# Kernel tuning notes

Measured on AMD Instinct MI355X. Metric: run time of the kernel, lower is better.

## Reference

```python
import jax, jax.numpy as jnp
import numpy as np

V = 50257   # vocab_size
BLOCK = 1024
D = 768     # n_embd
H = 12      # n_head
L = 2       # n_layer
B = 4
T = 1024
EPS = 1e-5


def _ln(x, g, b):
    mu = jnp.mean(x, axis=-1, keepdims=True)
    var = jnp.var(x, axis=-1, keepdims=True)
    return (x - mu) * jax.lax.rsqrt(var + EPS) * g + b


def setup_inputs() -> dict:
    key = jax.random.key(0)
    ks = jax.random.split(key, 10)
    def n(k, shape, std=0.02):
        return jax.random.normal(k, shape, jnp.float32) * std
    proj_std = (2 * L) ** -0.5  # set_scale init in the torch code
    return dict(
        idx=jax.random.randint(ks[0], (B, T), 0, V),
        layer_num=0,
        wte=n(ks[1], (V, D)),
        wpe=n(ks[2], (BLOCK, D)),
        ln1_g=jnp.ones((L, D)), ln1_b=jnp.zeros((L, D)),
        attn_w=n(ks[3], (L, D, 3 * D)), attn_b=jnp.zeros((L, 3 * D)),
        proj_w=n(ks[4], (L, D, D), proj_std), proj_b=jnp.zeros((L, D)),
        ln2_g=jnp.ones((L, D)), ln2_b=jnp.zeros((L, D)),
        fc_w=n(ks[5], (L, D, 4 * D)), fc_b=jnp.zeros((L, 4 * D)),
        fc2_w=n(ks[6], (L, 4 * D, D), proj_std), fc2_b=jnp.zeros((L, D)),
        lnf_g=jnp.ones((D,)), lnf_b=jnp.zeros((D,)),
        lm_w=n(ks[7], (D, V)),
    )


def _gpt(idx, wte, wpe, ln1_g, ln1_b, attn_w, attn_b, proj_w, proj_b,
         ln2_g, ln2_b, fc_w, fc_b, fc2_w, fc2_b, lnf_g, lnf_b, lm_w):
    b, t = idx.shape
    hd = D // H
    x = wte[idx] + wpe[:t]                      # [B,T,D]
    causal = jnp.tril(jnp.ones((t, t), bool))   # [T,T]
    for l in range(L):
        h = _ln(x, ln1_g[l], ln1_b[l])
        qkv = h @ attn_w[l] + attn_b[l]          # [B,T,3D]
        q, k, v = jnp.split(qkv, 3, axis=-1)
        q = q.reshape(b, t, H, hd)
        k = k.reshape(b, t, H, hd)
        v = v.reshape(b, t, H, hd)
        att = jnp.einsum('bqhd,bkhd->bhqk', q, k) * (1.0 / np.sqrt(hd))
        att = jnp.where(causal, att, -jnp.inf)
        att = jax.nn.softmax(att, axis=-1)
        y = jnp.einsum('bhqk,bkhd->bqhd', att, v).reshape(b, t, D)
        x = x + (y @ proj_w[l] + proj_b[l])
        h2 = _ln(x, ln2_g[l], ln2_b[l])
        h2 = jax.nn.gelu(h2 @ fc_w[l] + fc_b[l], approximate=True)  # tanh GELU
        x = x + (h2 @ fc2_w[l] + fc2_b[l])
    x = _ln(x, lnf_g, lnf_b)
    return x @ lm_w                             # [B,T,V] logits


def reference(idx, layer_num, wte, wpe, ln1_g, ln1_b, attn_w, attn_b,
              proj_w, proj_b, ln2_g, ln2_b, fc_w, fc_b, fc2_w, fc2_b,
              lnf_g, lnf_b, lm_w):
    # layer_num is unused in the forward math (pipeline-stage bookkeeping)
    return _gpt(idx, wte, wpe, ln1_g, ln1_b, attn_w, attn_b, proj_w, proj_b,
                ln2_g, ln2_b, fc_w, fc_b, fc2_w, fc2_b, lnf_g, lnf_b, lm_w)
```

## Files before the change

kernel.cpp:

```cpp
#include <hip/hip_runtime.h>
#include <hip/hip_bf16.h>
#include <cstdint>
#include <cstddef>

typedef __bf16 bf16_t;
typedef __bf16 bf16x8 __attribute__((ext_vector_type(8)));
typedef float f32x4 __attribute__((ext_vector_type(4)));

#define GLB_AS(p) ((__attribute__((address_space(1))) void*)(void*)(p))
#define LDS_AS(p) ((__attribute__((address_space(3))) void*)(p))

__device__ __forceinline__ float wave_red_sum(float v) {
#pragma unroll
  for (int o = 1; o < 64; o <<= 1) v += __shfl_xor(v, o, 64);
  return v;
}

__device__ __forceinline__ float gelu_tanh(float v) {
  float c = 0.7978845608028654f * (v + 0.044715f * v * v * v);
  return 0.5f * v * (1.0f + tanhf(c));
}

__global__ __launch_bounds__(256) void embed_k(const int* __restrict__ idx,
                                               const float* __restrict__ wte,
                                               const float* __restrict__ wpe,
                                               float* __restrict__ x) {
  const int m = blockIdx.x;
  const int tid = threadIdx.x;
  const int tok = idx[m];
  const int t = m & 1023;
#pragma unroll
  for (int i = 0; i < 3; ++i) {
    const int d = tid + i * 256;
    x[(size_t)m * 768 + d] = wte[(size_t)tok * 768 + d] + wpe[(size_t)t * 768 + d];
  }
}

__global__ __launch_bounds__(256) void ln_k(const float* __restrict__ x,
                                            const float* __restrict__ g,
                                            const float* __restrict__ b,
                                            bf16_t* __restrict__ out) {
  const int row = blockIdx.x;
  const int tid = threadIdx.x;
  const float* xr = x + (size_t)row * 768;
  float v0 = xr[tid], v1 = xr[tid + 256], v2 = xr[tid + 512];
  float s = v0 + v1 + v2;
  float q = v0 * v0 + v1 * v1 + v2 * v2;
  s = wave_red_sum(s);
  q = wave_red_sum(q);
  __shared__ float sm[8];
  const int wave = tid >> 6, lane = tid & 63;
  if (lane == 0) { sm[wave] = s; sm[4 + wave] = q; }
  __syncthreads();
  s = sm[0] + sm[1] + sm[2] + sm[3];
  q = sm[4] + sm[5] + sm[6] + sm[7];
  const float mu = s * (1.0f / 768.0f);
  const float var = q * (1.0f / 768.0f) - mu * mu;
  const float rs = rsqrtf(var + 1e-5f);
  bf16_t* orow = out + (size_t)row * 768;
#pragma unroll
  for (int i = 0; i < 3; ++i) {
    const int d = tid + i * 256;
    const float v = (i == 0 ? v0 : (i == 1 ? v1 : v2));
    orow[d] = (bf16_t)((v - mu) * rs * g[d] + b[d]);
  }
}

__global__ __launch_bounds__(256) void transp_k(const float* __restrict__ W,
                                                bf16_t* __restrict__ WT,
                                                int K, int N, int Npad) {
  __shared__ float tile[32][33];
  const int n0 = blockIdx.x * 32, k0 = blockIdx.y * 32;
  const int tx = threadIdx.x, ty = threadIdx.y;
#pragma unroll
  for (int i = 0; i < 4; ++i) {
    const int k = k0 + ty + i * 8, n = n0 + tx;
    tile[ty + i * 8][tx] = (k < K && n < N) ? W[(size_t)k * N + n] : 0.0f;
  }
  __syncthreads();
#pragma unroll
  for (int i = 0; i < 4; ++i) {
    const int n = n0 + ty + i * 8, k = k0 + tx;
    if (n < Npad && k < K) WT[(size_t)n * K + k] = (bf16_t)tile[tx][ty + i * 8];
  }
}

__global__ __launch_bounds__(256) void vtr_k(const bf16_t* __restrict__ qkv,
                                             bf16_t* __restrict__ vt) {
  __shared__ bf16_t tile[64][72];
  const int bh = blockIdx.y;
  const int h = bh % 12, b = bh / 12;
  const int t0 = blockIdx.x * 64;
  const int tx = threadIdx.x & 63;
  const int wv = threadIdx.x >> 6;
#pragma unroll
  for (int i = 0; i < 16; ++i) {
    const int r = wv * 16 + i;
    tile[r][tx] = qkv[(size_t)(b * 1024 + t0 + r) * 2304 + 1536 + h * 64 + tx];
  }
  __syncthreads();
#pragma unroll
  for (int i = 0; i < 16; ++i) {
    const int d = wv * 16 + i;
    vt[((size_t)bh * 64 + d) * 1024 + t0 + tx] = tile[tx][d];
  }
}

template <int EPI>
__global__ __launch_bounds__(256) void gemm_bt(const bf16_t* __restrict__ A,
                                               const bf16_t* __restrict__ BT,
                                               const float* __restrict__ bias,
                                               void* __restrict__ outp,
                                               float* __restrict__ resid,
                                               int M, int N, int K, int Nout) {
  __shared__ __align__(16) bf16_t As[128 * 32];
  __shared__ __align__(16) bf16_t Bs[128 * 32];
  const int tid = threadIdx.x;
  const int lane = tid & 63, wave = tid >> 6;

  const int nmblk = M >> 7;
  const int nwg = gridDim.x;
  const int flat = blockIdx.x;
  const int xcd = flat & 7, rest = flat >> 3;
  const int q8 = nwg >> 3, r8 = nwg & 7;
  const int wgid = (xcd < r8 ? xcd * (q8 + 1) : r8 * (q8 + 1) + (xcd - r8) * q8) + rest;
  const int m0 = (wgid % nmblk) * 128;
  const int n0 = (wgid / nmblk) * 128;

  const int wr = wave >> 1, wc = wave & 1;
  const int fr = lane & 15, fq = lane >> 4;
  const int se = tid * 8;
  const int srow = se >> 5, scol = se & 31;
  const int wvbase = wave * 512;
  f32x4 acc[4][4] = {};

  for (int k0 = 0; k0 < K; k0 += 32) {
#pragma unroll
    for (int r = 0; r < 2; ++r) {
      __builtin_amdgcn_global_load_lds(
          GLB_AS(&A[(size_t)(m0 + srow + r * 64) * K + k0 + scol]),
          LDS_AS(&As[wvbase + r * 2048]), 16, 0, 0);
      __builtin_amdgcn_global_load_lds(
          GLB_AS(&BT[(size_t)(n0 + srow + r * 64) * K + k0 + scol]),
          LDS_AS(&Bs[wvbase + r * 2048]), 16, 0, 0);
    }
    __syncthreads();
    bf16x8 a[4], b[4];
#pragma unroll
    for (int i = 0; i < 4; ++i) {
      a[i] = *(const bf16x8*)(&As[(wr * 64 + i * 16 + fr) * 32 + fq * 8]);
      b[i] = *(const bf16x8*)(&Bs[(wc * 64 + i * 16 + fr) * 32 + fq * 8]);
    }
#pragma unroll
    for (int i = 0; i < 4; ++i)
#pragma unroll
      for (int j = 0; j < 4; ++j)
        acc[i][j] = __builtin_amdgcn_mfma_f32_16x16x32_bf16(a[i], b[j], acc[i][j], 0, 0, 0);
    __syncthreads();
  }

#pragma unroll
  for (int i = 0; i < 4; ++i) {
#pragma unroll
    for (int j = 0; j < 4; ++j) {
      const int r0 = m0 + wr * 64 + i * 16 + fq * 4;
      const int c = n0 + wc * 64 + j * 16 + fr;
      float bv = 0.0f;
      if constexpr (EPI != 3) bv = bias[c];
#pragma unroll
      for (int e = 0; e < 4; ++e) {
        const int r = r0 + e;
        float v = acc[i][j][e] + bv;
        if constexpr (EPI == 0) {
          ((bf16_t*)outp)[(size_t)r * N + c] = (bf16_t)v;
        } else if constexpr (EPI == 1) {
          ((bf16_t*)outp)[(size_t)r * N + c] = (bf16_t)gelu_tanh(v);
        } else if constexpr (EPI == 2) {
          resid[(size_t)r * N + c] += v;
        } else {
          if (c < Nout) ((float*)outp)[(size_t)r * Nout + c] = v;
        }
      }
    }
  }
}

__global__ __launch_bounds__(256) void fattn_k(const bf16_t* __restrict__ qkv,
                                               const bf16_t* __restrict__ vt,
                                               bf16_t* __restrict__ y) {
  __shared__ bf16_t Pl[4][16][40];
  const int wave = threadIdx.x >> 6, lane = threadIdx.x & 63;
  const int wid = blockIdx.x * 4 + wave;
  const int qt = wid & 63;
  const int bh = wid >> 6;
  const int h = bh % 12, b = bh / 12;
  const int fr = lane & 15, fq = lane >> 4;

  const bf16_t* qrow = qkv + (size_t)(b * 1024 + qt * 16 + fr) * 2304 + h * 64;
  const bf16x8 qf0 = *(const bf16x8*)(qrow + fq * 8);
  const bf16x8 qf1 = *(const bf16x8*)(qrow + 32 + fq * 8);

  const bf16_t* kbase = qkv + (size_t)b * 1024 * 2304 + 768 + h * 64 + fq * 8;
  const bf16_t* vbase = vt + ((size_t)bh * 64 + fr) * 1024 + fq * 8;

  f32x4 o[4] = {};
  float mrun[4], lrun[4];
#pragma unroll
  for (int e = 0; e < 4; ++e) { mrun[e] = -1e30f; lrun[e] = 0.0f; }

  const int qg = qt * 16 + fq * 4;
  const int kv_end = qt * 16 + 16;

  for (int kv0 = 0; kv0 < kv_end; kv0 += 32) {
    f32x4 s0 = {}, s1 = {};
    {
      const bf16_t* k0p = kbase + (size_t)(kv0 + fr) * 2304;
      const bf16_t* k1p = kbase + (size_t)(kv0 + 16 + fr) * 2304;
      const bf16x8 kf00 = *(const bf16x8*)(k0p);
      const bf16x8 kf01 = *(const bf16x8*)(k0p + 32);
      const bf16x8 kf10 = *(const bf16x8*)(k1p);
      const bf16x8 kf11 = *(const bf16x8*)(k1p + 32);
      s0 = __builtin_amdgcn_mfma_f32_16x16x32_bf16(qf0, kf00, s0, 0, 0, 0);
      s0 = __builtin_amdgcn_mfma_f32_16x16x32_bf16(qf1, kf01, s0, 0, 0, 0);
      s1 = __builtin_amdgcn_mfma_f32_16x16x32_bf16(qf0, kf10, s1, 0, 0, 0);
      s1 = __builtin_amdgcn_mfma_f32_16x16x32_bf16(qf1, kf11, s1, 0, 0, 0);
    }
    float v0[4], v1[4];
#pragma unroll
    for (int e = 0; e < 4; ++e) {
      v0[e] = (kv0 + fr <= qg + e) ? s0[e] * 0.125f : -1e30f;
      v1[e] = (kv0 + 16 + fr <= qg + e) ? s1[e] * 0.125f : -1e30f;
    }
    float p0[4], p1[4];
#pragma unroll
    for (int e = 0; e < 4; ++e) {
      float mx = fmaxf(v0[e], v1[e]);
      mx = fmaxf(mx, __shfl_xor(mx, 1, 64));
      mx = fmaxf(mx, __shfl_xor(mx, 2, 64));
      mx = fmaxf(mx, __shfl_xor(mx, 4, 64));
      mx = fmaxf(mx, __shfl_xor(mx, 8, 64));
      const float mnew = fmaxf(mrun[e], mx);
      p0[e] = __expf(v0[e] - mnew);
      p1[e] = __expf(v1[e] - mnew);
      float rs = p0[e] + p1[e];
      rs += __shfl_xor(rs, 1, 64);
      rs += __shfl_xor(rs, 2, 64);
      rs += __shfl_xor(rs, 4, 64);
      rs += __shfl_xor(rs, 8, 64);
      const float alpha = __expf(mrun[e] - mnew);
      lrun[e] = lrun[e] * alpha + rs;
      mrun[e] = mnew;
#pragma unroll
      for (int db = 0; db < 4; ++db) o[db][e] *= alpha;
    }
#pragma unroll
    for (int e = 0; e < 4; ++e) {
      Pl[wave][fq * 4 + e][fr] = (bf16_t)p0[e];
      Pl[wave][fq * 4 + e][16 + fr] = (bf16_t)p1[e];
    }
    asm volatile("s_waitcnt lgkmcnt(0)" ::: "memory");
    const bf16x8 pf = *(const bf16x8*)(&Pl[wave][fr][fq * 8]);
#pragma unroll
    for (int db = 0; db < 4; ++db) {
      const bf16x8 vf = *(const bf16x8*)(vbase + (size_t)db * 16 * 1024 + kv0);
      o[db] = __builtin_amdgcn_mfma_f32_16x16x32_bf16(pf, vf, o[db], 0, 0, 0);
    }
  }

#pragma unroll
  for (int db = 0; db < 4; ++db) {
#pragma unroll
    for (int e = 0; e < 4; ++e) {
      const int q = qt * 16 + fq * 4 + e;
      const int d = db * 16 + fr;
      y[(size_t)(b * 1024 + q) * 768 + h * 64 + d] = (bf16_t)(o[db][e] / lrun[e]);
    }
  }
}

extern "C" void kernel_launch(void* const* d_in, const int* in_sizes, int n_in,
                              void* d_out, int out_size, void* d_ws, size_t ws_size,
                              hipStream_t stream) {
  constexpr int Bb = 4, T = 1024, Lg = 2, Vr = 50257, Vp = 50304;
  constexpr int M = Bb * T;

  const int* idx = (const int*)d_in[0];
  const float* wte = (const float*)d_in[2];
  const float* wpe = (const float*)d_in[3];
  const float* ln1_g = (const float*)d_in[4];
  const float* ln1_b = (const float*)d_in[5];
  const float* attn_w = (const float*)d_in[6];
  const float* attn_b = (const float*)d_in[7];
  const float* proj_w = (const float*)d_in[8];
  const float* proj_b = (const float*)d_in[9];
  const float* ln2_g = (const float*)d_in[10];
  const float* ln2_b = (const float*)d_in[11];
  const float* fc_w = (const float*)d_in[12];
  const float* fc_b = (const float*)d_in[13];
  const float* fc2_w = (const float*)d_in[14];
  const float* fc2_b = (const float*)d_in[15];
  const float* lnf_g = (const float*)d_in[16];
  const float* lnf_b = (const float*)d_in[17];
  const float* lm_w = (const float*)d_in[18];
  float* out = (float*)d_out;

  char* wp = (char*)d_ws;
  auto take = [&](size_t n) { char* p = wp; wp += (n + 255) & ~(size_t)255; return p; };
  bf16_t* WqkvT = (bf16_t*)take((size_t)Lg * 2304 * 768 * 2);
  bf16_t* WprojT = (bf16_t*)take((size_t)Lg * 768 * 768 * 2);
  bf16_t* WfcT = (bf16_t*)take((size_t)Lg * 3072 * 768 * 2);
  bf16_t* Wfc2T = (bf16_t*)take((size_t)Lg * 768 * 3072 * 2);
  bf16_t* WlmT = (bf16_t*)take((size_t)Vp * 768 * 2);
  float* xb = (float*)take((size_t)M * 768 * 4);
  bf16_t* hb = (bf16_t*)take((size_t)M * 768 * 2);
  bf16_t* qkvb = (bf16_t*)take((size_t)M * 2304 * 2);
  bf16_t* yb = (bf16_t*)take((size_t)M * 768 * 2);
  bf16_t* actb = (bf16_t*)take((size_t)M * 3072 * 2);
  bf16_t* vtb = (bf16_t*)take((size_t)M * 768 * 2);

  const dim3 tb(32, 8);
  for (int l = 0; l < Lg; ++l) {
    transp_k<<<dim3(2304 / 32, 768 / 32), tb, 0, stream>>>(
        attn_w + (size_t)l * 768 * 2304, WqkvT + (size_t)l * 2304 * 768, 768, 2304, 2304);
    transp_k<<<dim3(768 / 32, 768 / 32), tb, 0, stream>>>(
        proj_w + (size_t)l * 768 * 768, WprojT + (size_t)l * 768 * 768, 768, 768, 768);
    transp_k<<<dim3(3072 / 32, 768 / 32), tb, 0, stream>>>(
        fc_w + (size_t)l * 768 * 3072, WfcT + (size_t)l * 3072 * 768, 768, 3072, 3072);
    transp_k<<<dim3(768 / 32, 3072 / 32), tb, 0, stream>>>(
        fc2_w + (size_t)l * 3072 * 768, Wfc2T + (size_t)l * 768 * 3072, 3072, 768, 768);
  }
  transp_k<<<dim3(Vp / 32, 768 / 32), tb, 0, stream>>>(lm_w, WlmT, 768, Vr, Vp);

  embed_k<<<M, 256, 0, stream>>>(idx, wte, wpe, xb);

  for (int l = 0; l < Lg; ++l) {
    ln_k<<<M, 256, 0, stream>>>(xb, ln1_g + l * 768, ln1_b + l * 768, hb);
    gemm_bt<0><<<(M / 128) * (2304 / 128), 256, 0, stream>>>(
        hb, WqkvT + (size_t)l * 2304 * 768, attn_b + l * 2304, qkvb, nullptr,
        M, 2304, 768, 2304);
    vtr_k<<<dim3(T / 64, Bb * 12), 256, 0, stream>>>(qkvb, vtb);
    fattn_k<<<(Bb * 12 * 64) / 4, 256, 0, stream>>>(qkvb, vtb, yb);
    gemm_bt<2><<<(M / 128) * (768 / 128), 256, 0, stream>>>(
        yb, WprojT + (size_t)l * 768 * 768, proj_b + l * 768, nullptr, xb,
        M, 768, 768, 768);
    ln_k<<<M, 256, 0, stream>>>(xb, ln2_g + l * 768, ln2_b + l * 768, hb);
    gemm_bt<1><<<(M / 128) * (3072 / 128), 256, 0, stream>>>(
        hb, WfcT + (size_t)l * 3072 * 768, fc_b + l * 3072, actb, nullptr,
        M, 3072, 768, 3072);
    gemm_bt<2><<<(M / 128) * (768 / 128), 256, 0, stream>>>(
        actb, Wfc2T + (size_t)l * 768 * 3072, fc2_b + l * 768, nullptr, xb,
        M, 768, 3072, 768);
  }
  ln_k<<<M, 256, 0, stream>>>(xb, lnf_g, lnf_b, hb);
  gemm_bt<3><<<(M / 128) * (Vp / 128), 256, 0, stream>>>(
      hb, WlmT, nullptr, out, nullptr, M, Vp, 768, Vr);
}
```

Baseline: 1.355 ms.

## Add persistent 256x256 GEMM with 4-stage async LDS pipeline for QKV, FC, LM head

```diff
diff --git a/kernel.cpp b/kernel.cpp
--- a/kernel.cpp
+++ b/kernel.cpp
@@ -20,6 +20,13 @@
   float c = 0.7978845608028654f * (v + 0.044715f * v * v * v);
   return 0.5f * v * (1.0f + tanhf(c));
 }
+
+__device__ __forceinline__ f32x4 mfma16(f32x4 a, f32x4 b, f32x4 c) {
+  return __builtin_amdgcn_mfma_f32_16x16x32_bf16(
+      __builtin_bit_cast(bf16x8, a), __builtin_bit_cast(bf16x8, b), c, 0, 0, 0);
+}
+
+__device__ __forceinline__ int swz(int off) { return off ^ ((off >> 3) & 0x30); }
 
 __global__ __launch_bounds__(256) void embed_k(const int* __restrict__ idx,
                                                const float* __restrict__ wte,
@@ -107,6 +114,146 @@
 }
 
 template <int EPI>
+__global__ __launch_bounds__(512, 2) void gemm256p(const bf16_t* __restrict__ A,
+                                                   const bf16_t* __restrict__ BT,
+                                                   const float* __restrict__ bias,
+                                                   void* __restrict__ outp,
+                                                   int M, int N, int K, int Nout,
+                                                   int ntiles) {
+  __shared__ __align__(16) char lds[131072];
+  const int tid = threadIdx.x;
+  const int lane = tid & 63, wave = tid >> 6;
+  const int wr = wave >> 2, wc = wave & 3;
+  const int fr = lane & 15, fq = lane >> 4;
+
+  const int nmblk = M >> 8;
+  const int G = gridDim.x;
+  const int flat = blockIdx.x;
+  const int xcd = flat & 7, rest = flat >> 3;
+  const int q8 = G >> 3, r8 = G & 7;
+  const int bid = (xcd < r8 ? xcd * (q8 + 1) : r8 * (q8 + 1) + (xcd - r8) * q8) + rest;
+  const int qt = ntiles / G, rt = ntiles % G;
+  const int tstart = bid * qt + (bid < rt ? bid : rt);
+  const int cnt = qt + (bid < rt ? 1 : 0);
+  if (cnt == 0) return;
+  const int NT = K >> 5;
+  const int gEnd = cnt * NT;
+
+  int srow[2], scb[2];
+#pragma unroll
+  for (int u = 0; u < 2; ++u) {
+    const int s = swz(u * 8192 + tid * 16);
+    srow[u] = s >> 6;
+    scb[u] = s & 63;
+  }
+  const char* Abase = (const char*)A;
+  const char* Bbase = (const char*)BT;
+
+  auto stage4 = [&](int buf, int m0x, int n0x, int tauK) {
+#pragma unroll
+    for (int u = 0; u < 2; ++u) {
+      const char* srcA = Abase + ((size_t)(m0x + srow[u]) * K + tauK * 32) * 2 + scb[u];
+      __builtin_amdgcn_global_load_lds(GLB_AS(srcA),
+          LDS_AS(&lds[buf * 32768 + u * 8192 + wave * 1024]), 16, 0, 0);
+      const char* srcB = Bbase + ((size_t)(n0x + srow[u]) * K + tauK * 32) * 2 + scb[u];
+      __builtin_amdgcn_global_load_lds(GLB_AS(srcB),
+          LDS_AS(&lds[buf * 32768 + 16384 + u * 8192 + wave * 1024]), 16, 0, 0);
+    }
+  };
+
+  const int swzA0 = swz((wr * 128 + fr) * 64 + fq * 16);
+  const int swzB0 = 16384 + swz((wc * 64 + fr) * 64 + fq * 16);
+
+  int m0 = (tstart % nmblk) << 8, n0 = (tstart / nmblk) << 8;
+  int m3 = m0, n3 = n0, t3;
+  auto adv = [&](int& mx, int& nx, int& tx) {
+    if (++tx == NT) { tx = 0; mx += 256; if (mx >= M) { mx = 0; nx += 256; } }
+  };
+
+  f32x4 acc[8][4] = {};
+  f32x4 Xa[8], Xb[4], Ya[8], Yb[4];
+
+  {
+    int ms = m0, ns = n0, ts = 0;
+    stage4(0, ms, ns, ts); adv(ms, ns, ts);
+    stage4(1, ms, ns, ts); adv(ms, ns, ts);
+    stage4(2, ms, ns, ts); adv(ms, ns, ts);
+    m3 = ms; n3 = ns; t3 = ts;
+  }
+  asm volatile("s_waitcnt vmcnt(8)" ::: "memory");
+  __builtin_amdgcn_s_barrier();
+  __builtin_amdgcn_sched_barrier(0);
+#pragma unroll
+  for (int i = 0; i < 8; ++i) Xa[i] = *(const f32x4*)(&lds[swzA0 + i * 1024]);
+#pragma unroll
+  for (int j = 0; j < 4; ++j) Xb[j] = *(const f32x4*)(&lds[swzB0 + j * 1024]);
+
+  int g = 0;
+
+#define GSTEP(CA, CB, NA, NB)                                                          \
+  {                                                                                    \
+    if (g + 2 < gEnd) { asm volatile("s_waitcnt vmcnt(4)" ::: "memory"); }             \
+    else              { asm volatile("s_waitcnt vmcnt(0)" ::: "memory"); }             \
+    __builtin_amdgcn_s_barrier();                                                      \
+    __builtin_amdgcn_sched_barrier(0);                                                 \
+    if (g + 1 < gEnd) {                                                                \
+      const int bb1 = ((g + 1) & 3) << 15;                                             \
+      _Pragma("unroll")                                                                \
+      for (int i = 0; i < 8; ++i) NA[i] = *(const f32x4*)(&lds[bb1 + swzA0 + i * 1024]); \
+      _Pragma("unroll")                                                                \
+      for (int j = 0; j < 4; ++j) NB[j] = *(const f32x4*)(&lds[bb1 + swzB0 + j * 1024]); \
+      asm volatile("s_waitcnt lgkmcnt(12)" ::: "memory");                              \
+    } else {                                                                           \
+      asm volatile("s_waitcnt lgkmcnt(0)" ::: "memory");                               \
+    }                                                                                  \
+    __builtin_amdgcn_sched_barrier(0);                                                 \
+    if (g + 3 < gEnd) { stage4((g + 3) & 3, m3, n3, t3); adv(m3, n3, t3); }            \
+    __builtin_amdgcn_s_setprio(1);                                                     \
+    _Pragma("unroll")                                                                  \
+    for (int i = 0; i < 8; ++i)                                                        \
+      _Pragma("unroll")                                                                \
+      for (int j = 0; j < 4; ++j) acc[i][j] = mfma16(CA[i], CB[j], acc[i][j]);         \
+    __builtin_amdgcn_s_setprio(0);                                                     \
+    ++g;                                                                               \
+  }
+
+  for (int t = 0; t < cnt; ++t) {
+    for (int k2 = 0; k2 < NT; k2 += 2) {
+      GSTEP(Xa, Xb, Ya, Yb);
+      GSTEP(Ya, Yb, Xa, Xb);
+    }
+#pragma unroll
+    for (int i8 = 0; i8 < 8; ++i8) {
+#pragma unroll
+      for (int j4 = 0; j4 < 4; ++j4) {
+        const int r0 = m0 + wr * 128 + i8 * 16 + fq * 4;
+        const int c = n0 + wc * 64 + j4 * 16 + fr;
+        float bv = 0.0f;
+        if constexpr (EPI != 3) bv = bias[c];
+#pragma unroll
+        for (int e = 0; e < 4; ++e) {
+          const int r = r0 + e;
+          float v = acc[i8][j4][e] + bv;
+          if constexpr (EPI == 0) {
+            ((bf16_t*)outp)[(size_t)r * N + c] = (bf16_t)v;
+          } else if constexpr (EPI == 1) {
+            ((bf16_t*)outp)[(size_t)r * N + c] = (bf16_t)gelu_tanh(v);
+          } else {
+            if (c < Nout) ((float*)outp)[(size_t)r * Nout + c] = v;
+          }
+        }
+      }
+    }
+#pragma unroll
+    for (int i8 = 0; i8 < 8; ++i8)
+#pragma unroll
+      for (int j4 = 0; j4 < 4; ++j4) acc[i8][j4] = (f32x4){0.0f, 0.0f, 0.0f, 0.0f};
+    m0 += 256; if (m0 >= M) { m0 = 0; n0 += 256; }
+  }
+#undef GSTEP
+}
+
+template <int EPI>
 __global__ __launch_bounds__(256) void gemm_bt(const bf16_t* __restrict__ A,
                                                const bf16_t* __restrict__ BT,
                                                const float* __restrict__ bias,
@@ -165,21 +312,11 @@
     for (int j = 0; j < 4; ++j) {
       const int r0 = m0 + wr * 64 + i * 16 + fq * 4;
       const int c = n0 + wc * 64 + j * 16 + fr;
-      float bv = 0.0f;
-      if constexpr (EPI != 3) bv = bias[c];
+      const float bv = bias[c];
 #pragma unroll
       for (int e = 0; e < 4; ++e) {
         const int r = r0 + e;
-        float v = acc[i][j][e] + bv;
-        if constexpr (EPI == 0) {
-          ((bf16_t*)outp)[(size_t)r * N + c] = (bf16_t)v;
-        } else if constexpr (EPI == 1) {
-          ((bf16_t*)outp)[(size_t)r * N + c] = (bf16_t)gelu_tanh(v);
-        } else if constexpr (EPI == 2) {
-          resid[(size_t)r * N + c] += v;
-        } else {
-          if (c < Nout) ((float*)outp)[(size_t)r * Nout + c] = v;
-        }
+        resid[(size_t)r * N + c] += acc[i][j][e] + bv;
       }
     }
   }
@@ -281,7 +418,7 @@
 extern "C" void kernel_launch(void* const* d_in, const int* in_sizes, int n_in,
                               void* d_out, int out_size, void* d_ws, size_t ws_size,
                               hipStream_t stream) {
-  constexpr int Bb = 4, T = 1024, Lg = 2, Vr = 50257, Vp = 50304;
+  constexpr int Bb = 4, T = 1024, Lg = 2, Vr = 50257, Vp = 50432;
   constexpr int M = Bb * T;
 
   const int* idx = (const int*)d_in[0];
@@ -335,23 +472,23 @@
 
   for (int l = 0; l < Lg; ++l) {
     ln_k<<<M, 256, 0, stream>>>(xb, ln1_g + l * 768, ln1_b + l * 768, hb);
-    gemm_bt<0><<<(M / 128) * (2304 / 128), 256, 0, stream>>>(
-        hb, WqkvT + (size_t)l * 2304 * 768, attn_b + l * 2304, qkvb, nullptr,
-        M, 2304, 768, 2304);
+    gemm256p<0><<<(M / 256) * (2304 / 256), 512, 0, stream>>>(
+        hb, WqkvT + (size_t)l * 2304 * 768, attn_b + l * 2304, qkvb,
+        M, 2304, 768, 2304, (M / 256) * (2304 / 256));
     vtr_k<<<dim3(T / 64, Bb * 12), 256, 0, stream>>>(qkvb, vtb);
     fattn_k<<<(Bb * 12 * 64) / 4, 256, 0, stream>>>(qkvb, vtb, yb);
     gemm_bt<2><<<(M / 128) * (768 / 128), 256, 0, stream>>>(
         yb, WprojT + (size_t)l * 768 * 768, proj_b + l * 768, nullptr, xb,
         M, 768, 768, 768);
     ln_k<<<M, 256, 0, stream>>>(xb, ln2_g + l * 768, ln2_b + l * 768, hb);
-    gemm_bt<1><<<(M / 128) * (3072 / 128), 256, 0, stream>>>(
-        hb, WfcT + (size_t)l * 3072 * 768, fc_b + l * 3072, actb, nullptr,
-        M, 3072, 768, 3072);
+    gemm256p<1><<<(M / 256) * (3072 / 256), 512, 0, stream>>>(
+        hb, WfcT + (size_t)l * 3072 * 768, fc_b + l * 3072, actb,
+        M, 3072, 768, 3072, (M / 256) * (3072 / 256));
     gemm_bt<2><<<(M / 128) * (768 / 128), 256, 0, stream>>>(
         actb, Wfc2T + (size_t)l * 768 * 3072, fc2_b + l * 768, nullptr, xb,
         M, 768, 3072, 768);
   }
   ln_k<<<M, 256, 0, stream>>>(xb, lnf_g, lnf_b, hb);
-  gemm_bt<3><<<(M / 128) * (Vp / 128), 256, 0, stream>>>(
-      hb, WlmT, nullptr, out, nullptr, M, Vp, 768, Vr);
-}
+  gemm256p<3><<<512, 512, 0, stream>>>(
+      hb, WlmT, nullptr, out, M, Vp, 768, Vr, (M / 256) * (Vp / 256));
+}
```

Result: faster. 1.260 ms (-7.0%).
